# Kernel optimization log

Hardware: AMD Instinct MI355X
Metric: run time of the kernel (lower is better)

Reference implementation:

```python
import jax, jax.numpy as jnp
import numpy as np

EMBED_DIM = 1024
NUM_HEADS = 16
HEAD_DIM = EMBED_DIM // NUM_HEADS
TGT_LEN, BSZ = 2048, 4


def setup_inputs() -> dict:
    key = jax.random.key(0)
    ks = jax.random.split(key, 12)
    s = 1.0 / np.sqrt(EMBED_DIM)
    inp = {
        "query": jax.random.normal(ks[0], (TGT_LEN, BSZ, EMBED_DIM), jnp.float32),
        "key": jax.random.normal(ks[1], (TGT_LEN, BSZ, EMBED_DIM), jnp.float32),
        "value": jax.random.normal(ks[2], (TGT_LEN, BSZ, EMBED_DIM), jnp.float32),
        # nn.Linear weights: [out, in], y = x @ W.T + b
        "Wq": jax.random.normal(ks[3], (EMBED_DIM, EMBED_DIM), jnp.float32) * s,
        "bq": jax.random.normal(ks[4], (EMBED_DIM,), jnp.float32) * s,
        "Wk": jax.random.normal(ks[5], (EMBED_DIM, EMBED_DIM), jnp.float32) * s,
        "bk": jax.random.normal(ks[6], (EMBED_DIM,), jnp.float32) * s,
        "Wv": jax.random.normal(ks[7], (EMBED_DIM, EMBED_DIM), jnp.float32) * s,
        "bv": jax.random.normal(ks[8], (EMBED_DIM,), jnp.float32) * s,
        "Wo": jax.random.normal(ks[9], (EMBED_DIM, EMBED_DIM), jnp.float32) * s,
        "bo": jax.random.normal(ks[10], (EMBED_DIM,), jnp.float32) * s,
    }
    return inp


def _split_heads(x, seq_len, bsz):
    # [S, B, E] -> [B*H, S, Dh]
    return x.reshape(seq_len, bsz * NUM_HEADS, HEAD_DIM).transpose(1, 0, 2)


def reference(query, key, value, Wq, bq, Wk, bk, Wv, bv, Wo, bo):
    tgt_len, bsz, embed_dim = query.shape
    src_len = key.shape[0]
    q = query @ Wq.T + bq
    k = key @ Wk.T + bk
    v = value @ Wv.T + bv
    q = _split_heads(q, tgt_len, bsz)   # [B*H, T, Dh]
    k = _split_heads(k, src_len, bsz)   # [B*H, S, Dh]
    v = _split_heads(v, src_len, bsz)   # [B*H, S, Dh]
    scale = 1.0 / np.sqrt(HEAD_DIM).astype(np.float32)
    attn_weights = jnp.einsum('btd,bsd->bts', q, k) * scale  # [B*H, T, S]
    attn_weights = jax.nn.softmax(attn_weights, axis=-1)
    attn = jnp.einsum('bts,bsd->btd', attn_weights, v)       # [B*H, T, Dh]
    attn = attn.transpose(1, 0, 2).reshape(tgt_len, bsz, embed_dim)
    return attn @ Wo.T + bo
```

## Files before the change

kernel.cpp:

```cpp
#include <hip/hip_runtime.h>
#include <stdint.h>

#define TGT 2048
#define BSZQ 4
#define EMB 1024
#define NHEAD 16
#define DH 64
#define BH 64
#define MROWS 8192

using short8 = __attribute__((ext_vector_type(8))) short;
using f32x4  = __attribute__((ext_vector_type(4))) float;
using u32x2  = __attribute__((ext_vector_type(2))) unsigned int;
typedef unsigned short u16;
typedef unsigned int u32;

#define QSCALE 0.18033688011112042f

__device__ __forceinline__ u16 f2bf(float f) {
  union { float f; u32 u; } v; v.f = f;
  return (u16)((v.u + 0x7fffu + ((v.u >> 16) & 1u)) >> 16);
}
__device__ __forceinline__ u32 packbf(float a, float b) {
  union { float f; u32 u; } x, y; x.f = a; y.f = b;
  return __builtin_amdgcn_perm(y.u + 0x8000u, x.u + 0x8000u, 0x07060302u);
}
__device__ __forceinline__ f32x4 mfma16(short8 a, short8 b, f32x4 c) {
  return __builtin_amdgcn_mfma_f32_16x16x32_bf16(a, b, c, 0, 0, 0);
}
__device__ __forceinline__ void gload_lds16(const u16* g, u16* l) {
  __builtin_amdgcn_global_load_lds((const __attribute__((address_space(1))) void*)g,
                                   (__attribute__((address_space(3))) void*)l,
                                   16, 0, 0);
}

__global__ __launch_bounds__(256)
void cvt3(const float* __restrict__ a, const float* __restrict__ b, const float* __restrict__ c,
          u16* __restrict__ oa, u16* __restrict__ ob, u16* __restrict__ oc)
{
  const float* s; u16* d;
  if (blockIdx.y == 0) { s = a; d = oa; }
  else if (blockIdx.y == 1) { s = b; d = ob; }
  else { s = c; d = oc; }
  const int i = (blockIdx.x * 256 + threadIdx.x) * 8;
  float4 v0 = *(const float4*)(s + i);
  float4 v1 = *(const float4*)(s + i + 4);
  union { u16 h[8]; short8 v; } r;
  r.h[0] = f2bf(v0.x); r.h[1] = f2bf(v0.y); r.h[2] = f2bf(v0.z); r.h[3] = f2bf(v0.w);
  r.h[4] = f2bf(v1.x); r.h[5] = f2bf(v1.y); r.h[6] = f2bf(v1.z); r.h[7] = f2bf(v1.w);
  *(short8*)(d + i) = r.v;
}
__global__ __launch_bounds__(256)
void cvt4(const float* __restrict__ a, const float* __restrict__ b,
          const float* __restrict__ c, const float* __restrict__ e,
          u16* __restrict__ oa, u16* __restrict__ ob, u16* __restrict__ oc, u16* __restrict__ oe)
{
  const float* s; u16* d;
  if (blockIdx.y == 0) { s = a; d = oa; }
  else if (blockIdx.y == 1) { s = b; d = ob; }
  else if (blockIdx.y == 2) { s = c; d = oc; }
  else { s = e; d = oe; }
  const int i = (blockIdx.x * 256 + threadIdx.x) * 8;
  float4 v0 = *(const float4*)(s + i);
  float4 v1 = *(const float4*)(s + i + 4);
  union { u16 h[8]; short8 v; } r;
  r.h[0] = f2bf(v0.x); r.h[1] = f2bf(v0.y); r.h[2] = f2bf(v0.z); r.h[3] = f2bf(v0.w);
  r.h[4] = f2bf(v1.x); r.h[5] = f2bf(v1.y); r.h[6] = f2bf(v1.z); r.h[7] = f2bf(v1.w);
  *(short8*)(d + i) = r.v;
}

__device__ __forceinline__
void gemm_body(const u16* __restrict__ A, const u16* __restrict__ W,
               const float* __restrict__ bias, void* __restrict__ outp,
               u16* As, u16* Bs, int mode, int m0, int n0)
{
  const int tid = threadIdx.x;
  const int wave = tid >> 6, lane = tid & 63;
  const int col16 = lane & 15, quad = lane >> 4;
  const int wr = (wave >> 1) * 64;
  const int wc = (wave & 1) * 64;
  const int sr = lane >> 3;
  const int sg = (lane & 7) ^ sr;
  const int fk = col16 & 7;

#define GSTAGE(K0) do { \
  _Pragma("unroll") for (int s_ = 0; s_ < 4; ++s_) \
    gload_lds16(A + (size_t)(m0 + wave * 32 + s_ * 8 + sr) * EMB + (K0) + sg * 8, \
                &As[(wave * 32 + s_ * 8) * 64]); \
  _Pragma("unroll") for (int s_ = 0; s_ < 4; ++s_) \
    gload_lds16(W + (size_t)(n0 + wave * 32 + s_ * 8 + sr) * EMB + (K0) + sg * 8, \
                &Bs[(wave * 32 + s_ * 8) * 64]); \
} while (0)

  f32x4 acc[4][4];
#pragma unroll
  for (int i = 0; i < 4; ++i)
#pragma unroll
    for (int j = 0; j < 4; ++j) acc[i][j] = (f32x4)0.0f;

  for (int kt = 0; kt < EMB / 64; ++kt) {
    if (kt) __syncthreads();
    GSTAGE(kt * 64);
    __syncthreads();
    short8 af[4][2], bfr[4][2];
#pragma unroll
    for (int kk = 0; kk < 2; ++kk) {
#pragma unroll
      for (int i = 0; i < 4; ++i)
        af[i][kk] = *(const short8*)&As[(wr + i * 16 + col16) * 64
                                        + (((kk * 4 + quad) ^ fk) << 3)];
#pragma unroll
      for (int j = 0; j < 4; ++j)
        bfr[j][kk] = *(const short8*)&Bs[(wc + j * 16 + col16) * 64
                                         + (((kk * 4 + quad) ^ fk) << 3)];
    }
#pragma unroll
    for (int i = 0; i < 4; ++i)
#pragma unroll
      for (int j = 0; j < 4; ++j) {
        acc[i][j] = mfma16(af[i][0], bfr[j][0], acc[i][j]);
        acc[i][j] = mfma16(af[i][1], bfr[j][1], acc[i][j]);
      }
  }
#undef GSTAGE

  const int rowb = quad * 4;
#pragma unroll
  for (int i = 0; i < 4; ++i) {
#pragma unroll
    for (int j = 0; j < 4; ++j) {
      const int gn = n0 + wc + j * 16 + col16;
      const float bia = bias[gn];
      const int h = gn >> 6, d = gn & 63;
#pragma unroll
      for (int r = 0; r < 4; ++r) {
        const int gm = m0 + wr + i * 16 + rowb + r;
        float val = acc[i][j][r] + bia;
        const int t = gm >> 2, b = gm & 3;
        if (mode == 0) {
          ((u16*)outp)[((size_t)(b * NHEAD + h) * TGT + t) * DH + d] = f2bf(val * QSCALE);
        } else if (mode == 1) {
          ((u16*)outp)[((size_t)(b * NHEAD + h) * TGT + t) * DH + d] = f2bf(val);
        } else if (mode == 2) {
          const int p = (t & ~63) + ((t & 15) << 2) + ((t >> 4) & 3);
          ((u16*)outp)[((size_t)(b * NHEAD + h) * DH + d) * TGT + p] = f2bf(val);
        } else {
          ((float*)outp)[(size_t)gm * EMB + gn] = val;
        }
      }
    }
  }
}

__global__ __launch_bounds__(256, 4)
void gemm_qkv(const u16* __restrict__ qb, const u16* __restrict__ kb, const u16* __restrict__ vb,
              const u16* __restrict__ wq, const u16* __restrict__ wk, const u16* __restrict__ wv,
              const float* __restrict__ bq, const float* __restrict__ bk, const float* __restrict__ bv,
              u16* __restrict__ qh, u16* __restrict__ kh, u16* __restrict__ vtp)
{
  __shared__ u16 As[8192];
  __shared__ u16 Bs[8192];
  const int lin = ((int)blockIdx.z * 64 + blockIdx.y) * 8 + blockIdx.x;
  const int swz = (lin & 7) * 192 + (lin >> 3);
  const int n0 = (swz & 7) * 128;
  const int tmp = swz >> 3;
  const int m0 = (tmp & 63) * 128;
  const int z = tmp >> 6;
  const u16* A = (z == 0) ? qb : (z == 1) ? kb : vb;
  const u16* W = (z == 0) ? wq : (z == 1) ? wk : wv;
  const float* bias = (z == 0) ? bq : (z == 1) ? bk : bv;
  void* outp = (z == 0) ? (void*)qh : (z == 1) ? (void*)kh : (void*)vtp;
  gemm_body(A, W, bias, outp, As, Bs, z, m0, n0);
}

__global__ __launch_bounds__(256, 4)
void gemm_o(const u16* __restrict__ A, const u16* __restrict__ W,
            const float* __restrict__ bias, float* __restrict__ outp)
{
  __shared__ u16 As[8192];
  __shared__ u16 Bs[8192];
  const int lin = (int)blockIdx.y * 8 + blockIdx.x;
  const int swz = (lin & 7) * 64 + (lin >> 3);
  const int n0 = (swz & 7) * 128;
  const int m0 = (swz >> 3) * 128;
  gemm_body(A, W, bias, (void*)outp, As, Bs, 3, m0, n0);
}

__global__ __launch_bounds__(256, 3)
void flash_attn(const u16* __restrict__ qh, const u16* __restrict__ kh,
                const u16* __restrict__ vtp, u16* __restrict__ ao)
{
  __shared__ u16 Ks[2 * 64 * 64];
  __shared__ u16 Vs[2 * 64 * 64];
  __shared__ u16 Ps[128 * 64];

  const int tid = threadIdx.x;
  const int wave = tid >> 6, lane = tid & 63;
  const int col16 = lane & 15, quad = lane >> 4;
  const int id = blockIdx.x;
  const int bh = (id & 7) * 8 + (id >> 7);
  const int q0 = ((id >> 3) & 15) * 128;
  const int wq0 = q0 + wave * 32;

  const u16* qbase = qh + (size_t)bh * TGT * DH;
  const u16* kbase = kh + (size_t)bh * TGT * DH;
  const u16* vbase = vtp + (size_t)bh * DH * TGT;

  const int krl = lane >> 3;
  const int kgl = (lane & 7) ^ krl;
  const int vgl = (lane & 7) ^ krl;

#define STAGE(S0, B) do { \
  _Pragma("unroll") for (int t_ = 0; t_ < 2; ++t_) { \
    gload_lds16(kbase + (size_t)((S0) + t_ * 32 + wave * 8 + krl) * DH + kgl * 8, \
                &Ks[(B) * 4096 + (t_ * 32 + wave * 8) * 64]); \
    gload_lds16(vbase + (size_t)(t_ * 32 + wave * 8 + krl) * TGT + (S0) + vgl * 8, \
                &Vs[(B) * 4096 + (t_ * 32 + wave * 8) * 64]); \
  } } while (0)

  short8 qf[2][2];
#pragma unroll
  for (int i = 0; i < 2; ++i)
#pragma unroll
    for (int kk = 0; kk < 2; ++kk)
      qf[i][kk] = *(const short8*)(qbase + (size_t)(wq0 + i * 16 + col16) * DH + kk * 32 + quad * 8);

  f32x4 oacc[2][4];
  float lsum[2][4];
#pragma unroll
  for (int i = 0; i < 2; ++i)
#pragma unroll
    for (int j = 0; j < 4; ++j) oacc[i][j] = (f32x4)0.0f;
#pragma unroll
  for (int i = 0; i < 2; ++i)
#pragma unroll
    for (int r = 0; r < 4; ++r) lsum[i][r] = 0.0f;

  STAGE(0, 0);

  for (int st = 0; st < TGT / 64; ++st) {
    const int cb = st & 1;
    __syncthreads();
    if (st < TGT / 64 - 1) STAGE((st + 1) * 64, cb ^ 1);

    u32 pka[2][4][2];
#pragma unroll
    for (int jpL = 0; jpL < 2; ++jpL) {
      f32x4 s[2][2];
#pragma unroll
      for (int jh = 0; jh < 2; ++jh) {
        const int j = jpL * 2 + jh;
        const int R = j * 16 + col16;
        short8 kf0 = *(const short8*)&Ks[cb * 4096 + R * 64 + ((quad ^ (col16 & 7)) << 3)];
        short8 kf1 = *(const short8*)&Ks[cb * 4096 + R * 64 + (((quad + 4) ^ (col16 & 7)) << 3)];
#pragma unroll
        for (int i = 0; i < 2; ++i) {
          f32x4 t0 = mfma16(qf[i][0], kf0, (f32x4)0.0f);
          s[i][jh] = mfma16(qf[i][1], kf1, t0);
        }
      }
#pragma unroll
      for (int i = 0; i < 2; ++i)
#pragma unroll
        for (int r = 0; r < 4; ++r) {
          float p0 = __builtin_amdgcn_exp2f(s[i][0][r]);
          float p1 = __builtin_amdgcn_exp2f(s[i][1][r]);
          lsum[i][r] += p0 + p1;
          pka[i][r][jpL] = packbf(p0, p1);
        }
    }
#pragma unroll
    for (int i = 0; i < 2; ++i)
#pragma unroll
      for (int r = 0; r < 4; ++r) {
        const int row = wave * 32 + i * 16 + quad * 4 + r;
        u32x2 w2; w2[0] = pka[i][r][0]; w2[1] = pka[i][r][1];
        *(u32x2*)&Ps[row * 64 + (((col16 >> 1) ^ (row & 7)) << 3) + ((col16 & 1) << 2)] = w2;
      }
#pragma unroll
    for (int ks = 0; ks < 2; ++ks) {
      short8 pf[2];
#pragma unroll
      for (int i = 0; i < 2; ++i) {
        const int row = wave * 32 + i * 16 + col16;
        pf[i] = *(const short8*)&Ps[row * 64 + (((ks * 4 + quad) ^ (col16 & 7)) << 3)];
      }
#pragma unroll
      for (int jd = 0; jd < 4; ++jd) {
        const int d = jd * 16 + col16;
        short8 vf = *(const short8*)&Vs[cb * 4096 + d * 64
                                        + (((ks * 4 + quad) ^ (col16 & 7)) << 3)];
#pragma unroll
        for (int i = 0; i < 2; ++i)
          oacc[i][jd] = mfma16(pf[i], vf, oacc[i][jd]);
      }
    }
  }
#undef STAGE

#pragma unroll
  for (int i = 0; i < 2; ++i)
#pragma unroll
    for (int r = 0; r < 4; ++r) {
#pragma unroll
      for (int off = 1; off < 16; off <<= 1)
        lsum[i][r] += __shfl_xor(lsum[i][r], off, 64);
      lsum[i][r] = __builtin_amdgcn_rcpf(lsum[i][r]);
    }
  const int b = bh >> 4, h = bh & 15;
#pragma unroll
  for (int i = 0; i < 2; ++i)
#pragma unroll
    for (int jd = 0; jd < 4; ++jd)
#pragma unroll
      for (int r = 0; r < 4; ++r) {
        const int t = q0 + wave * 32 + i * 16 + quad * 4 + r;
        const int d = jd * 16 + col16;
        ao[((size_t)t * BSZQ + b) * EMB + h * DH + d] = f2bf(oacc[i][jd][r] * lsum[i][r]);
      }
}

extern "C" void kernel_launch(void* const* d_in, const int* in_sizes, int n_in,
                              void* d_out, int out_size, void* d_ws, size_t ws_size,
                              hipStream_t stream) {
  const float* query = (const float*)d_in[0];
  const float* key   = (const float*)d_in[1];
  const float* value = (const float*)d_in[2];
  const float* Wq = (const float*)d_in[3];
  const float* bq = (const float*)d_in[4];
  const float* Wk = (const float*)d_in[5];
  const float* bk = (const float*)d_in[6];
  const float* Wv = (const float*)d_in[7];
  const float* bv = (const float*)d_in[8];
  const float* Wo = (const float*)d_in[9];
  const float* bo = (const float*)d_in[10];

  const size_t BIG = (size_t)MROWS * EMB;
  const size_t WSZ = (size_t)EMB * EMB;
  u16* buf0 = (u16*)d_ws;
  u16* buf1 = buf0 + BIG;
  u16* buf2 = buf1 + BIG;
  u16* buf3 = buf2 + BIG;
  u16* wqb  = buf3 + BIG;
  u16* wkb  = wqb + WSZ;
  u16* wvb  = wkb + WSZ;
  u16* wob  = wvb + WSZ;
  u16* khs  = (u16*)d_out;
  u16* vts  = khs + BIG;

  cvt3<<<dim3(BIG / 2048, 3), 256, 0, stream>>>(query, key, value, buf0, buf1, buf2);
  cvt4<<<dim3(WSZ / 2048, 4), 256, 0, stream>>>(Wq, Wk, Wv, Wo, wqb, wkb, wvb, wob);

  gemm_qkv<<<dim3(EMB / 128, MROWS / 128, 3), 256, 0, stream>>>(
      buf0, buf1, buf2, wqb, wkb, wvb, bq, bk, bv,
      buf3 , khs , vts );

  flash_attn<<<1024, 256, 0, stream>>>(buf3, khs, vts, buf2);

  gemm_o<<<dim3(EMB / 128, MROWS / 128), 256, 0, stream>>>(buf2, wob, bo, (float*)d_out);
}
```

Baseline: 371.7 us.

## Keep softmax probabilities in registers by computing transposed scores, dropping LDS P round-trip

The QK^T MFMA now has its operands swapped so each lane holds scores laid out to match the A-operand fragment of the PV MFMA. The bf16-packed probabilities can then go straight into the second matmul, with no write to and read from shared memory. The V^T permutation in the QKV GEMM epilogue changes to match the new key ordering, and the row-sum reduction is reworked to use cross-quad shuffles plus a broadcast. Removing the Ps buffer cuts LDS use, so launch bounds go from 3 to 4 blocks per SM, at some risk of register pressure.

```diff
diff --git a/kernel.cpp b/kernel.cpp
--- a/kernel.cpp
+++ b/kernel.cpp
@@ -11,7 +11,6 @@
 
 using short8 = __attribute__((ext_vector_type(8))) short;
 using f32x4  = __attribute__((ext_vector_type(4))) float;
-using u32x2  = __attribute__((ext_vector_type(2))) unsigned int;
 typedef unsigned short u16;
 typedef unsigned int u32;
 
@@ -142,7 +141,7 @@
         } else if (mode == 1) {
           ((u16*)outp)[((size_t)(b * NHEAD + h) * TGT + t) * DH + d] = f2bf(val);
         } else if (mode == 2) {
-          const int p = (t & ~63) + ((t & 15) << 2) + ((t >> 4) & 3);
+          const int p = (t & ~63) + ((t & 12) << 2) + ((t & 48) >> 2) + (t & 3);
           ((u16*)outp)[((size_t)(b * NHEAD + h) * DH + d) * TGT + p] = f2bf(val);
         } else {
           ((float*)outp)[(size_t)gm * EMB + gn] = val;
@@ -186,13 +185,12 @@
   gemm_body(A, W, bias, (void*)outp, As, Bs, 3, m0, n0);
 }
 
-__global__ __launch_bounds__(256, 3)
+__global__ __launch_bounds__(256, 4)
 void flash_attn(const u16* __restrict__ qh, const u16* __restrict__ kh,
                 const u16* __restrict__ vtp, u16* __restrict__ ao)
 {
   __shared__ u16 Ks[2 * 64 * 64];
   __shared__ u16 Vs[2 * 64 * 64];
-  __shared__ u16 Ps[128 * 64];
 
   const int tid = threadIdx.x;
   const int wave = tid >> 6, lane = tid & 63;
@@ -208,13 +206,12 @@
 
   const int krl = lane >> 3;
   const int kgl = (lane & 7) ^ krl;
-  const int vgl = (lane & 7) ^ krl;
 
 #define STAGE(S0, B) do { \
   _Pragma("unroll") for (int t_ = 0; t_ < 2; ++t_) { \
     gload_lds16(kbase + (size_t)((S0) + t_ * 32 + wave * 8 + krl) * DH + kgl * 8, \
                 &Ks[(B) * 4096 + (t_ * 32 + wave * 8) * 64]); \
-    gload_lds16(vbase + (size_t)(t_ * 32 + wave * 8 + krl) * TGT + (S0) + vgl * 8, \
+    gload_lds16(vbase + (size_t)(t_ * 32 + wave * 8 + krl) * TGT + (S0) + kgl * 8, \
                 &Vs[(B) * 4096 + (t_ * 32 + wave * 8) * 64]); \
   } } while (0)
 
@@ -226,15 +223,13 @@
       qf[i][kk] = *(const short8*)(qbase + (size_t)(wq0 + i * 16 + col16) * DH + kk * 32 + quad * 8);
 
   f32x4 oacc[2][4];
-  float lsum[2][4];
-#pragma unroll
-  for (int i = 0; i < 2; ++i)
+  float lsum[2];
+#pragma unroll
+  for (int i = 0; i < 2; ++i) {
+    lsum[i] = 0.0f;
 #pragma unroll
     for (int j = 0; j < 4; ++j) oacc[i][j] = (f32x4)0.0f;
-#pragma unroll
-  for (int i = 0; i < 2; ++i)
-#pragma unroll
-    for (int r = 0; r < 4; ++r) lsum[i][r] = 0.0f;
+  }
 
   STAGE(0, 0);
 
@@ -243,70 +238,54 @@
     __syncthreads();
     if (st < TGT / 64 - 1) STAGE((st + 1) * 64, cb ^ 1);
 
-    u32 pka[2][4][2];
-#pragma unroll
-    for (int jpL = 0; jpL < 2; ++jpL) {
-      f32x4 s[2][2];
-#pragma unroll
-      for (int jh = 0; jh < 2; ++jh) {
-        const int j = jpL * 2 + jh;
-        const int R = j * 16 + col16;
-        short8 kf0 = *(const short8*)&Ks[cb * 4096 + R * 64 + ((quad ^ (col16 & 7)) << 3)];
-        short8 kf1 = *(const short8*)&Ks[cb * 4096 + R * 64 + (((quad + 4) ^ (col16 & 7)) << 3)];
+    u32 pka[4][2][2];
+#pragma unroll
+    for (int j = 0; j < 4; ++j) {
+      const int R = j * 16 + col16;
+      short8 kf0 = *(const short8*)&Ks[cb * 4096 + R * 64 + ((quad ^ (col16 & 7)) << 3)];
+      short8 kf1 = *(const short8*)&Ks[cb * 4096 + R * 64 + (((quad + 4) ^ (col16 & 7)) << 3)];
+#pragma unroll
+      for (int i = 0; i < 2; ++i) {
+        f32x4 t0 = mfma16(kf0, qf[i][0], (f32x4)0.0f);
+        f32x4 s  = mfma16(kf1, qf[i][1], t0);
+        float p0 = __builtin_amdgcn_exp2f(s[0]);
+        float p1 = __builtin_amdgcn_exp2f(s[1]);
+        float p2 = __builtin_amdgcn_exp2f(s[2]);
+        float p3 = __builtin_amdgcn_exp2f(s[3]);
+        lsum[i] += (p0 + p1) + (p2 + p3);
+        pka[j][i][0] = packbf(p0, p1);
+        pka[j][i][1] = packbf(p2, p3);
+      }
+    }
+#pragma unroll
+    for (int jd = 0; jd < 4; ++jd) {
+      const int d = jd * 16 + col16;
+#pragma unroll
+      for (int h = 0; h < 2; ++h) {
+        short8 vf = *(const short8*)&Vs[cb * 4096 + d * 64
+                                        + (((quad * 2 + h) ^ (d & 7)) << 3)];
 #pragma unroll
         for (int i = 0; i < 2; ++i) {
-          f32x4 t0 = mfma16(qf[i][0], kf0, (f32x4)0.0f);
-          s[i][jh] = mfma16(qf[i][1], kf1, t0);
+          union { u32 u[4]; short8 s8; } pa;
+          pa.u[0] = pka[2 * h][i][0];     pa.u[1] = pka[2 * h][i][1];
+          pa.u[2] = pka[2 * h + 1][i][0]; pa.u[3] = pka[2 * h + 1][i][1];
+          oacc[i][jd] = mfma16(pa.s8, vf, oacc[i][jd]);
         }
       }
-#pragma unroll
-      for (int i = 0; i < 2; ++i)
-#pragma unroll
-        for (int r = 0; r < 4; ++r) {
-          float p0 = __builtin_amdgcn_exp2f(s[i][0][r]);
-          float p1 = __builtin_amdgcn_exp2f(s[i][1][r]);
-          lsum[i][r] += p0 + p1;
-          pka[i][r][jpL] = packbf(p0, p1);
-        }
     }
-#pragma unroll
-    for (int i = 0; i < 2; ++i)
-#pragma unroll
-      for (int r = 0; r < 4; ++r) {
-        const int row = wave * 32 + i * 16 + quad * 4 + r;
-        u32x2 w2; w2[0] = pka[i][r][0]; w2[1] = pka[i][r][1];
-        *(u32x2*)&Ps[row * 64 + (((col16 >> 1) ^ (row & 7)) << 3) + ((col16 & 1) << 2)] = w2;
-      }
-#pragma unroll
-    for (int ks = 0; ks < 2; ++ks) {
-      short8 pf[2];
-#pragma unroll
-      for (int i = 0; i < 2; ++i) {
-        const int row = wave * 32 + i * 16 + col16;
-        pf[i] = *(const short8*)&Ps[row * 64 + (((ks * 4 + quad) ^ (col16 & 7)) << 3)];
-      }
-#pragma unroll
-      for (int jd = 0; jd < 4; ++jd) {
-        const int d = jd * 16 + col16;
-        short8 vf = *(const short8*)&Vs[cb * 4096 + d * 64
-                                        + (((ks * 4 + quad) ^ (col16 & 7)) << 3)];
-#pragma unroll
-        for (int i = 0; i < 2; ++i)
-          oacc[i][jd] = mfma16(pf[i], vf, oacc[i][jd]);
-      }
-    }
   }
 #undef STAGE
 
-#pragma unroll
-  for (int i = 0; i < 2; ++i)
-#pragma unroll
-    for (int r = 0; r < 4; ++r) {
-#pragma unroll
-      for (int off = 1; off < 16; off <<= 1)
-        lsum[i][r] += __shfl_xor(lsum[i][r], off, 64);
-      lsum[i][r] = __builtin_amdgcn_rcpf(lsum[i][r]);
-    }
+  float lrow[2][4];
+#pragma unroll
+  for (int i = 0; i < 2; ++i) {
+    float L = lsum[i];
+    L += __shfl_xor(L, 16, 64);
+    L += __shfl_xor(L, 32, 64);
+    L = __builtin_amdgcn_rcpf(L);
+#pragma unroll
+    for (int r = 0; r < 4; ++r) lrow[i][r] = __shfl(L, quad * 4 + r, 64);
+  }
   const int b = bh >> 4, h = bh & 15;
 #pragma unroll
   for (int i = 0; i < 2; ++i)
@@ -316,7 +295,7 @@
       for (int r = 0; r < 4; ++r) {
         const int t = q0 + wave * 32 + i * 16 + quad * 4 + r;
         const int d = jd * 16 + col16;
-        ao[((size_t)t * BSZQ + b) * EMB + h * DH + d] = f2bf(oacc[i][jd][r] * lsum[i][r]);
+        ao[((size_t)t * BSZQ + b) * EMB + h * DH + d] = f2bf(oacc[i][jd][r] * lrow[i][r]);
       }
 }
 
```

Result: faster. 360.2 us, median of 2 (-3.1%).
